# Performance work log

Hardware: AMD Instinct MI355X
Metric: run time of the kernel (lower is better)

The kernel has to match this reference:

```python
import jax, jax.numpy as jnp
import numpy as np


def setup_inputs() -> dict:
    key = jax.random.key(0)
    k1, k2, k3, k4 = jax.random.split(key, 4)
    B, T, C = 4, 2048, 1024
    x = jax.random.normal(k1, (B, T, C), dtype=jnp.float32)
    scale = 1.0 / np.sqrt(C)
    Wq = jax.random.normal(k2, (C, C), dtype=jnp.float32) * scale
    Wk = jax.random.normal(k3, (C, C), dtype=jnp.float32) * scale
    Wv = jax.random.normal(k4, (C, C), dtype=jnp.float32) * scale
    return {"x": x, "Wq": Wq, "Wk": Wk, "Wv": Wv}


def reference(x, Wq, Wk, Wv):
    # x: [B, T, C]; torch Linear(no bias): y = x @ W.T
    B, T, C = x.shape
    q = jnp.einsum('btc,dc->btd', x, Wq)
    k = jnp.einsum('btc,dc->btd', x, Wk)
    v = jnp.einsum('btc,dc->btd', x, Wv)
    scale = jnp.asarray(C, x.dtype) ** -0.5
    qk = jnp.einsum('bqd,bkd->bqk', q, k) * scale  # [B, T, T]
    causal = jnp.tril(jnp.ones((T, T), dtype=bool))
    qk = jnp.where(causal, qk, -jnp.inf)
    attn = jax.nn.softmax(qk, axis=-1)
    out = jnp.einsum('bqk,bkd->bqd', attn, v)
    return out
```

## Files before the change

kernel.cpp:

```cpp
#include <hip/hip_runtime.h>

typedef __attribute__((ext_vector_type(8))) short  short8;
typedef __attribute__((ext_vector_type(4))) short  short4v;
typedef __attribute__((ext_vector_type(4))) float  floatx4;

__device__ inline short f2bf(float f) {
    union { float f; unsigned u; } v; v.f = f;
    unsigned r = v.u + 0x7fffu + ((v.u >> 16) & 1u);
    return (short)(r >> 16);
}

typedef const __attribute__((address_space(1))) unsigned int* gp1_t;
typedef __attribute__((address_space(3))) unsigned int* lp3_t;

__device__ __attribute__((always_inline)) inline void gl_lds16(const short* g, short* l) {
    __builtin_amdgcn_global_load_lds((gp1_t)g, (lp3_t)l, 16, 0, 0);
}

#define MFMA_BF16 __builtin_amdgcn_mfma_f32_16x16x32_bf16

__device__ __attribute__((always_inline)) inline void gemm_bt_core(
    const short* __restrict__ Ag, const short* __restrict__ Bg,
    int lda, int ldb, int kmax,
    short* As, short* Bs, floatx4 acc[4][4])
{
    const int t    = threadIdx.x;
    const int srow = t >> 3;
    const int scol = (t & 7) * 8;
    const int lane = t & 63;
    const int wid  = t >> 6;
    const int wx   = wid & 1, wy = wid >> 1;
    const int lm   = lane & 15, lq = lane >> 4;

    for (int k0 = 0; k0 < kmax; k0 += 64) {
        __syncthreads();
#pragma unroll
        for (int i = 0; i < 4; ++i) {
            gl_lds16(Ag + (size_t)(i * 32 + srow) * lda + k0 + scol,
                     As + (i * 32 + srow) * 64 + scol);
            gl_lds16(Bg + (size_t)(i * 32 + srow) * ldb + k0 + scol,
                     Bs + (i * 32 + srow) * 64 + scol);
        }
        __syncthreads();

#pragma unroll
        for (int ks = 0; ks < 2; ++ks) {
            short8 af[4], bfr[4];
#pragma unroll
            for (int mi = 0; mi < 4; ++mi)
                af[mi] = *(const short8*)(As + (wy * 64 + mi * 16 + lm) * 64 + ks * 32 + lq * 8);
#pragma unroll
            for (int ni = 0; ni < 4; ++ni)
                bfr[ni] = *(const short8*)(Bs + (wx * 64 + ni * 16 + lm) * 64 + ks * 32 + lq * 8);
#pragma unroll
            for (int mi = 0; mi < 4; ++mi)
#pragma unroll
                for (int ni = 0; ni < 4; ++ni)
                    acc[mi][ni] = MFMA_BF16(af[mi], bfr[ni], acc[mi][ni], 0, 0, 0);
        }
    }
}

__global__ void cast_all(const float* __restrict__ x,
                         const float* __restrict__ Wq,
                         const float* __restrict__ Wk,
                         const float* __restrict__ Wv,
                         short* __restrict__ xb, short* __restrict__ wb,
                         float* __restrict__ lsum)
{
    size_t v = (size_t)blockIdx.x * 256 + threadIdx.x;
    const float* src; short* dst; size_t off;
    if (v < 2097152)      { src = x;  dst = xb;           off = v; }
    else if (v < 2359296) { src = Wq; dst = wb;           off = v - 2097152; }
    else if (v < 2621440) { src = Wk; dst = wb + 1048576; off = v - 2359296; }
    else if (v < 2883584) { src = Wv; dst = wb + 2097152; off = v - 2621440; }
    else if (v < 2885632) {
        floatx4 z = {0.f, 0.f, 0.f, 0.f};
        ((floatx4*)lsum)[v - 2883584] = z;
        return;
    } else return;
    floatx4 vv = ((const floatx4*)src)[off];
    short4v s;
#pragma unroll
    for (int e = 0; e < 4; ++e) s[e] = f2bf(vv[e]);
    ((short4v*)dst)[off] = s;
}

struct Q8Ctx {
    const short* Ag; const short* Bg;
    short *A0, *B0, *A1, *B1;
    int srow, scl, scg;
    int aB, bB, c0, c1;
};

#define LD_AF(SLOT, HI) do { _Pragma("unroll") \
    for (int mi_ = 0; mi_ < 4; ++mi_) { \
        af[mi_][0] = *(const short8*)((SLOT) + X.aB + (HI) + mi_ * 1024 + X.c0); \
        af[mi_][1] = *(const short8*)((SLOT) + X.aB + (HI) + mi_ * 1024 + X.c1); \
    } } while (0)

#define LD_BF(SLOT, N0) do { _Pragma("unroll") \
    for (int ni_ = 0; ni_ < 2; ++ni_) { \
        bf[(N0) + ni_][0] = *(const short8*)((SLOT) + X.bB + ((N0) + ni_) * 1024 + X.c0); \
        bf[(N0) + ni_][1] = *(const short8*)((SLOT) + X.bB + ((N0) + ni_) * 1024 + X.c1); \
    } } while (0)

#define MM_Q(MB, N0) do { _Pragma("unroll") \
    for (int mi_ = 0; mi_ < 4; ++mi_) { _Pragma("unroll") \
        for (int ni_ = 0; ni_ < 2; ++ni_) { \
            acc[(MB)+mi_][(N0)+ni_] = MFMA_BF16(af[mi_][0], bf[(N0)+ni_][0], acc[(MB)+mi_][(N0)+ni_], 0, 0, 0); \
            acc[(MB)+mi_][(N0)+ni_] = MFMA_BF16(af[mi_][1], bf[(N0)+ni_][1], acc[(MB)+mi_][(N0)+ni_], 0, 0, 0); \
        } } } while (0)

#define STAGE_HALF(DST, SRC, KOFS) do { \
    gl_lds16((SRC) + (size_t)(X.srow)      * 1024 + (KOFS) + X.scg, (DST) + (X.srow)      * 64 + X.scl); \
    gl_lds16((SRC) + (size_t)(64 + X.srow) * 1024 + (KOFS) + X.scg, (DST) + (64 + X.srow) * 64 + X.scl); \
    } while (0)

#define BARR  __builtin_amdgcn_s_barrier()
#define WLG0  asm volatile("s_waitcnt lgkmcnt(0)" ::: "memory")
#define WLG8  asm volatile("s_waitcnt lgkmcnt(8)" ::: "memory")
#define PRI1  __builtin_amdgcn_s_setprio(1)
#define PRI0  __builtin_amdgcn_s_setprio(0)

template<bool TAIL>
__device__ __attribute__((always_inline)) inline void iter8(
    const Q8Ctx& X, int kb, floatx4 acc[8][4])
{
    const int sk1 = kb + 64, sk2 = kb + 128, sk3 = kb + 192;
    short8 af[4][2], bf[4][2];

    LD_AF(X.A0, 0); LD_BF(X.B0, 0);
    STAGE_HALF(X.A1, X.Ag, sk1);
    WLG8;
    BARR; WLG0; PRI1; MM_Q(0, 0); PRI0; BARR;
    LD_BF(X.B0, 2);
    STAGE_HALF(X.A1 + 8192, X.Ag + 131072, sk1);
    BARR; WLG0; PRI1; MM_Q(0, 2); PRI0; BARR;
    LD_AF(X.A0, 4096);
    if (!TAIL) STAGE_HALF(X.B0, X.Bg, sk2);
    BARR; WLG0; PRI1; MM_Q(4, 2); PRI0; BARR;
    if (!TAIL) STAGE_HALF(X.B0 + 8192, X.Bg + 131072, sk2);
    BARR; PRI1; MM_Q(4, 0); PRI0;
    if (!TAIL) asm volatile("s_waitcnt vmcnt(4)" ::: "memory");
    else       asm volatile("s_waitcnt vmcnt(0)" ::: "memory");
    BARR;

    LD_AF(X.A1, 0); LD_BF(X.B1, 0);
    if (!TAIL) STAGE_HALF(X.A0, X.Ag, sk2);
    WLG8;
    BARR; WLG0; PRI1; MM_Q(0, 0); PRI0; BARR;
    LD_BF(X.B1, 2);
    if (!TAIL) STAGE_HALF(X.A0 + 8192, X.Ag + 131072, sk2);
    BARR; WLG0; PRI1; MM_Q(0, 2); PRI0; BARR;
    LD_AF(X.A1, 4096);
    if (!TAIL) STAGE_HALF(X.B1, X.Bg, sk3);
    BARR; WLG0; PRI1; MM_Q(4, 2); PRI0; BARR;
    if (!TAIL) STAGE_HALF(X.B1 + 8192, X.Bg + 131072, sk3);
    BARR; PRI1; MM_Q(4, 0); PRI0;
    if (!TAIL) asm volatile("s_waitcnt vmcnt(4)" ::: "memory");
    BARR;
}

__global__ __launch_bounds__(512, 2) void qkv_gemm8(
    const short* __restrict__ xb, const short* __restrict__ wb,
    short* __restrict__ qb, short* __restrict__ kb, short* __restrict__ vt)
{
    __shared__ short lds[65536];

    const int orig = blockIdx.x;
    const int tile = (orig & 7) * 48 + (orig >> 3);
    const int mt = tile & 31;
    const int nt = tile >> 5;
    const int m0 = mt * 256;

    const int t    = threadIdx.x;
    const int lane = t & 63;
    const int wid  = t >> 6;
    const int wy   = wid >> 2, wx = wid & 3;
    const int lm   = lane & 15, lq = lane >> 4;

    Q8Ctx X;
    X.Ag = xb + (size_t)m0 * 1024;
    X.Bg = wb + (size_t)(nt * 256) * 1024;
    X.A0 = lds;          X.B0 = lds + 16384;
    X.A1 = lds + 32768;  X.B1 = lds + 49152;
    X.srow = t >> 3;
    X.scl  = (t & 7) * 8;
    X.scg  = ((t & 7) ^ (X.srow & 7)) * 8;
    X.c0 = (lq ^ (lm & 7)) * 8;
    X.c1 = ((4 + lq) ^ (lm & 7)) * 8;
    X.aB = (wy * 128 + lm) * 64;
    X.bB = (wx * 64 + lm) * 64;

    floatx4 acc[8][4];
    floatx4 zero = {0.f, 0.f, 0.f, 0.f};
#pragma unroll
    for (int i = 0; i < 8; ++i)
#pragma unroll
        for (int j = 0; j < 4; ++j) acc[i][j] = zero;

    STAGE_HALF(X.A0,         X.Ag,          0);
    STAGE_HALF(X.A0 + 8192,  X.Ag + 131072, 0);
    STAGE_HALF(X.B0,         X.Bg,          0);
    STAGE_HALF(X.B0 + 8192,  X.Bg + 131072, 0);
    STAGE_HALF(X.B1,         X.Bg,          64);
    STAGE_HALF(X.B1 + 8192,  X.Bg + 131072, 64);
    asm volatile("s_waitcnt vmcnt(4)" ::: "memory");
    __builtin_amdgcn_s_barrier();

#pragma unroll 1
    for (int i = 0; i < 7; ++i)
        iter8<false>(X, i * 128, acc);
    iter8<true>(X, 7 * 128, acc);

    const int nglob = nt * 256;
    const int which = nglob >> 10;
    const int ncol  = (nglob & 1023) + wx * 64;
#pragma unroll
    for (int mi = 0; mi < 8; ++mi)
#pragma unroll
        for (int r = 0; r < 4; ++r) {
            const int row = m0 + wy * 128 + mi * 16 + lq * 4 + r;
#pragma unroll
            for (int ni = 0; ni < 4; ++ni) {
                const int col = ncol + ni * 16 + lm;
                const short bv = f2bf(acc[mi][ni][r]);
                if (which == 2) {
                    const int bb = row >> 11, tt = row & 2047;
                    vt[((size_t)bb * 1024 + col) * 2048 + tt] = bv;
                } else if (which == 1) {
                    kb[(size_t)row * 1024 + col] = bv;
                } else {
                    qb[(size_t)row * 1024 + col] = bv;
                }
            }
        }
}

__global__ __launch_bounds__(256, 3) void sqk_gemm(
    const short* __restrict__ qb, const short* __restrict__ kb,
    short* __restrict__ P, float* __restrict__ lsum)
{
    int idx = blockIdx.x;
    int i = 0;
    while ((i + 1) * (i + 2) / 2 <= idx) ++i;
    const int j = idx - i * (i + 1) / 2;
    const int b = blockIdx.y;

    __shared__ short As[128 * 64];
    __shared__ short Bs[128 * 64];

    floatx4 acc[4][4];
    floatx4 zero = {0.f, 0.f, 0.f, 0.f};
#pragma unroll
    for (int a = 0; a < 4; ++a)
#pragma unroll
        for (int c = 0; c < 4; ++c) acc[a][c] = zero;

    gemm_bt_core(qb + ((size_t)(b * 2048 + i * 128)) * 1024,
                 kb + ((size_t)(b * 2048 + j * 128)) * 1024,
                 1024, 1024, 1024, As, Bs, acc);

    const float sscl = 0.03125f * 1.44269504089f;
    const bool  diag = (i == j);
    const int lane = threadIdx.x & 63, wid = threadIdx.x >> 6;
    const int wx = wid & 1, wy = wid >> 1, lm = lane & 15, lq = lane >> 4;

#pragma unroll
    for (int mi = 0; mi < 4; ++mi)
#pragma unroll
        for (int r = 0; r < 4; ++r) {
            const int lrow = wy * 64 + mi * 16 + lq * 4 + r;
            const int grow = i * 128 + lrow;
            short* prow = P + ((size_t)b * 2048 + grow) * 2048 + j * 128;
            float rsum = 0.f;
#pragma unroll
            for (int ni = 0; ni < 4; ++ni) {
                const int lcol = wx * 64 + ni * 16 + lm;
                float p = exp2f(acc[mi][ni][r] * sscl);
                if (diag && lcol > lrow) p = 0.f;
                rsum += p;
                prow[lcol] = f2bf(p);
            }
#pragma unroll
            for (int off = 1; off < 16; off <<= 1) rsum += __shfl_xor(rsum, off);
            if (lm == 0) atomicAdd(lsum + b * 2048 + grow, rsum);
        }
}

__global__ __launch_bounds__(256, 3) void pv_gemm(
    const short* __restrict__ P, const short* __restrict__ vt,
    const float* __restrict__ lsum, float* __restrict__ out)
{
    const int x  = blockIdx.x;
    const int pr = blockIdx.y;
    const int b  = blockIdx.z;
    const int n0 = x * 64;

    __shared__ short As[128 * 64];
    __shared__ short Bs[64 * 64];

    const int t    = threadIdx.x;
    const int srow = t >> 3;
    const int scol = (t & 7) * 8;
    const int lane = t & 63;
    const int wid  = t >> 6;
    const int wx   = wid & 1, wy = wid >> 1;
    const int lm   = lane & 15, lq = lane >> 4;

    const short* Bg = vt + ((size_t)b * 1024 + n0) * 2048;

#pragma unroll
    for (int phase = 0; phase < 2; ++phase) {
        const int i    = phase ? (15 - pr) : pr;
        const int kmax = (i + 1) * 128;
        const short* Ag = P + ((size_t)b * 2048 + i * 128) * 2048;

        floatx4 acc[4][2];
        floatx4 zero = {0.f, 0.f, 0.f, 0.f};
#pragma unroll
        for (int a = 0; a < 4; ++a)
#pragma unroll
            for (int c = 0; c < 2; ++c) acc[a][c] = zero;

        for (int k0 = 0; k0 < kmax; k0 += 64) {
            __syncthreads();
#pragma unroll
            for (int q = 0; q < 4; ++q)
                gl_lds16(Ag + (size_t)(q * 32 + srow) * 2048 + k0 + scol,
                         As + (q * 32 + srow) * 64 + scol);
#pragma unroll
            for (int q = 0; q < 2; ++q)
                gl_lds16(Bg + (size_t)(q * 32 + srow) * 2048 + k0 + scol,
                         Bs + (q * 32 + srow) * 64 + scol);
            __syncthreads();

#pragma unroll
            for (int ks = 0; ks < 2; ++ks) {
                short8 af[4], bfr[2];
#pragma unroll
                for (int mi = 0; mi < 4; ++mi)
                    af[mi] = *(const short8*)(As + (wy * 64 + mi * 16 + lm) * 64 + ks * 32 + lq * 8);
#pragma unroll
                for (int ni = 0; ni < 2; ++ni)
                    bfr[ni] = *(const short8*)(Bs + (wx * 32 + ni * 16 + lm) * 64 + ks * 32 + lq * 8);
#pragma unroll
                for (int mi = 0; mi < 4; ++mi)
#pragma unroll
                    for (int ni = 0; ni < 2; ++ni)
                        acc[mi][ni] = MFMA_BF16(af[mi], bfr[ni], acc[mi][ni], 0, 0, 0);
            }
        }

#pragma unroll
        for (int mi = 0; mi < 4; ++mi)
#pragma unroll
            for (int r = 0; r < 4; ++r) {
                const int grow = b * 2048 + i * 128 + wy * 64 + mi * 16 + lq * 4 + r;
                const float li = 1.0f / lsum[grow];
#pragma unroll
                for (int ni = 0; ni < 2; ++ni)
                    out[(size_t)grow * 1024 + n0 + wx * 32 + ni * 16 + lm] =
                        acc[mi][ni][r] * li;
            }
    }
}

extern "C" void kernel_launch(void* const* d_in, const int* in_sizes, int n_in,
                              void* d_out, int out_size, void* d_ws, size_t ws_size,
                              hipStream_t stream)
{
    (void)in_sizes; (void)n_in; (void)out_size; (void)ws_size;
    const float* x  = (const float*)d_in[0];
    const float* Wq = (const float*)d_in[1];
    const float* Wk = (const float*)d_in[2];
    const float* Wv = (const float*)d_in[3];
    float* out = (float*)d_out;

    char* base = (char*)d_ws;
    short* xb   = (short*)(base);
    short* wb   = (short*)(base + 16777216);
    short* qb   = (short*)(base + 23068672);
    short* kb   = (short*)(base + 39845888);
    short* vt   = (short*)(base + 56623104);
    short* P    = (short*)(base + 73400320);
    float* lsum = (float*)(base + 107954176);

    cast_all<<<11272, 256, 0, stream>>>(x, Wq, Wk, Wv, xb, wb, lsum);
    qkv_gemm8<<<dim3(384), 512, 0, stream>>>(xb, wb, qb, kb, vt);
    sqk_gemm<<<dim3(136, 4), 256, 0, stream>>>(qb, kb, P, lsum);
    pv_gemm<<<dim3(16, 8, 4), 256, 0, stream>>>(P, vt, lsum, out);
}
```

Baseline: 282.5 us.

## Split-K PV GEMM with atomics and rework QKV GEMM A-tile prefetch schedule

The PV GEMM now uses 128x128 output tiles via the shared gemm_bt_core. Long causal row blocks (i>=8) are split into two K halves that combine with float atomicAdd, and short rows are written directly. The lower half of the output is zeroed in the cast kernel so the atomics have a clean target. The QKV GEMM schedule is also reordered so A tiles are prefetched two stages ahead alongside B, with the waitcnt values adjusted to match. This trades more atomic traffic and an extra output-zeroing pass for better load balance and larger tiles.

```diff
diff --git a/kernel.cpp b/kernel.cpp
--- a/kernel.cpp
+++ b/kernel.cpp
@@ -66,7 +66,7 @@
                          const float* __restrict__ Wk,
                          const float* __restrict__ Wv,
                          short* __restrict__ xb, short* __restrict__ wb,
-                         float* __restrict__ lsum)
+                         float* __restrict__ lsum, float* __restrict__ out)
 {
     size_t v = (size_t)blockIdx.x * 256 + threadIdx.x;
     const float* src; short* dst; size_t off;
@@ -78,6 +78,12 @@
         floatx4 z = {0.f, 0.f, 0.f, 0.f};
         ((floatx4*)lsum)[v - 2883584] = z;
         return;
+    } else if (v < 3934208) {
+        size_t u = v - 2885632;
+        size_t bb = u >> 18, r = u & 262143;
+        floatx4 z = {0.f, 0.f, 0.f, 0.f};
+        ((floatx4*)out)[(bb * 2048 + 1024) * 256 + r] = z;
+        return;
     } else return;
     floatx4 vv = ((const floatx4*)src)[off];
     short4v s;
@@ -123,42 +129,46 @@
 #define PRI1  __builtin_amdgcn_s_setprio(1)
 #define PRI0  __builtin_amdgcn_s_setprio(0)
 
-template<bool TAIL>
-__device__ __attribute__((always_inline)) inline void iter8(
+template<int MODE>
+__device__ __attribute__((always_inline)) inline void iter8d(
     const Q8Ctx& X, int kb, floatx4 acc[8][4])
 {
-    const int sk1 = kb + 64, sk2 = kb + 128, sk3 = kb + 192;
+    const int sk2 = kb + 128, sk3 = kb + 192;
     short8 af[4][2], bf[4][2];
 
     LD_AF(X.A0, 0); LD_BF(X.B0, 0);
-    STAGE_HALF(X.A1, X.Ag, sk1);
     WLG8;
     BARR; WLG0; PRI1; MM_Q(0, 0); PRI0; BARR;
     LD_BF(X.B0, 2);
-    STAGE_HALF(X.A1 + 8192, X.Ag + 131072, sk1);
     BARR; WLG0; PRI1; MM_Q(0, 2); PRI0; BARR;
     LD_AF(X.A0, 4096);
-    if (!TAIL) STAGE_HALF(X.B0, X.Bg, sk2);
+    if (MODE == 0) STAGE_HALF(X.B0, X.Bg, sk2);
     BARR; WLG0; PRI1; MM_Q(4, 2); PRI0; BARR;
-    if (!TAIL) STAGE_HALF(X.B0 + 8192, X.Bg + 131072, sk2);
+    if (MODE == 0) {
+        STAGE_HALF(X.B0 + 8192, X.Bg + 131072, sk2);
+        STAGE_HALF(X.A0,        X.Ag,          sk2);
+    }
     BARR; PRI1; MM_Q(4, 0); PRI0;
-    if (!TAIL) asm volatile("s_waitcnt vmcnt(4)" ::: "memory");
-    else       asm volatile("s_waitcnt vmcnt(0)" ::: "memory");
+    if (MODE == 0) asm volatile("s_waitcnt vmcnt(6)" ::: "memory");
+    else           asm volatile("s_waitcnt vmcnt(0)" ::: "memory");
     BARR;
 
     LD_AF(X.A1, 0); LD_BF(X.B1, 0);
-    if (!TAIL) STAGE_HALF(X.A0, X.Ag, sk2);
+    if (MODE == 0) STAGE_HALF(X.A0 + 8192, X.Ag + 131072, sk2);
     WLG8;
     BARR; WLG0; PRI1; MM_Q(0, 0); PRI0; BARR;
     LD_BF(X.B1, 2);
-    if (!TAIL) STAGE_HALF(X.A0 + 8192, X.Ag + 131072, sk2);
     BARR; WLG0; PRI1; MM_Q(0, 2); PRI0; BARR;
     LD_AF(X.A1, 4096);
-    if (!TAIL) STAGE_HALF(X.B1, X.Bg, sk3);
+    if (MODE == 0) STAGE_HALF(X.B1, X.Bg, sk3);
     BARR; WLG0; PRI1; MM_Q(4, 2); PRI0; BARR;
-    if (!TAIL) STAGE_HALF(X.B1 + 8192, X.Bg + 131072, sk3);
+    if (MODE == 0) {
+        STAGE_HALF(X.B1 + 8192, X.Bg + 131072, sk3);
+        STAGE_HALF(X.A1,        X.Ag,          sk3);
+        STAGE_HALF(X.A1 + 8192, X.Ag + 131072, sk3);
+    }
     BARR; PRI1; MM_Q(4, 0); PRI0;
-    if (!TAIL) asm volatile("s_waitcnt vmcnt(4)" ::: "memory");
+    if (MODE == 0) asm volatile("s_waitcnt vmcnt(8)" ::: "memory");
     BARR;
 }
 
@@ -200,19 +210,21 @@
 #pragma unroll
         for (int j = 0; j < 4; ++j) acc[i][j] = zero;
 
+    STAGE_HALF(X.B0,         X.Bg,          0);
+    STAGE_HALF(X.B0 + 8192,  X.Bg + 131072, 0);
     STAGE_HALF(X.A0,         X.Ag,          0);
     STAGE_HALF(X.A0 + 8192,  X.Ag + 131072, 0);
-    STAGE_HALF(X.B0,         X.Bg,          0);
-    STAGE_HALF(X.B0 + 8192,  X.Bg + 131072, 0);
     STAGE_HALF(X.B1,         X.Bg,          64);
     STAGE_HALF(X.B1 + 8192,  X.Bg + 131072, 64);
-    asm volatile("s_waitcnt vmcnt(4)" ::: "memory");
+    STAGE_HALF(X.A1,         X.Ag,          64);
+    STAGE_HALF(X.A1 + 8192,  X.Ag + 131072, 64);
+    asm volatile("s_waitcnt vmcnt(8)" ::: "memory");
     __builtin_amdgcn_s_barrier();
 
 #pragma unroll 1
     for (int i = 0; i < 7; ++i)
-        iter8<false>(X, i * 128, acc);
-    iter8<true>(X, 7 * 128, acc);
+        iter8d<0>(X, i * 128, acc);
+    iter8d<1>(X, 7 * 128, acc);
 
     const int nglob = nt * 256;
     const int which = nglob >> 10;
@@ -293,78 +305,55 @@
     const short* __restrict__ P, const short* __restrict__ vt,
     const float* __restrict__ lsum, float* __restrict__ out)
 {
-    const int x  = blockIdx.x;
-    const int pr = blockIdx.y;
+    const int id = blockIdx.x;
+    const int x  = blockIdx.y;
     const int b  = blockIdx.z;
-    const int n0 = x * 64;
+    int i, kbeg, kend;
+    bool single;
+    if (id < 8) {
+        i = id; kbeg = 0; kend = (i + 1) * 128; single = true;
+    } else {
+        const int id2 = id - 8;
+        i = 8 + (id2 >> 1);
+        const int c = id2 & 1;
+        kbeg = c ? 1024 : 0;
+        kend = c ? (i + 1) * 128 : 1024;
+        single = false;
+    }
+    const int n0 = x * 128;
 
     __shared__ short As[128 * 64];
-    __shared__ short Bs[64 * 64];
-
-    const int t    = threadIdx.x;
-    const int srow = t >> 3;
-    const int scol = (t & 7) * 8;
-    const int lane = t & 63;
-    const int wid  = t >> 6;
-    const int wx   = wid & 1, wy = wid >> 1;
-    const int lm   = lane & 15, lq = lane >> 4;
-
-    const short* Bg = vt + ((size_t)b * 1024 + n0) * 2048;
-
-#pragma unroll
-    for (int phase = 0; phase < 2; ++phase) {
-        const int i    = phase ? (15 - pr) : pr;
-        const int kmax = (i + 1) * 128;
-        const short* Ag = P + ((size_t)b * 2048 + i * 128) * 2048;
-
-        floatx4 acc[4][2];
-        floatx4 zero = {0.f, 0.f, 0.f, 0.f};
-#pragma unroll
-        for (int a = 0; a < 4; ++a)
-#pragma unroll
-            for (int c = 0; c < 2; ++c) acc[a][c] = zero;
-
-        for (int k0 = 0; k0 < kmax; k0 += 64) {
-            __syncthreads();
-#pragma unroll
-            for (int q = 0; q < 4; ++q)
-                gl_lds16(Ag + (size_t)(q * 32 + srow) * 2048 + k0 + scol,
-                         As + (q * 32 + srow) * 64 + scol);
-#pragma unroll
-            for (int q = 0; q < 2; ++q)
-                gl_lds16(Bg + (size_t)(q * 32 + srow) * 2048 + k0 + scol,
-                         Bs + (q * 32 + srow) * 64 + scol);
-            __syncthreads();
-
-#pragma unroll
-            for (int ks = 0; ks < 2; ++ks) {
-                short8 af[4], bfr[2];
-#pragma unroll
-                for (int mi = 0; mi < 4; ++mi)
-                    af[mi] = *(const short8*)(As + (wy * 64 + mi * 16 + lm) * 64 + ks * 32 + lq * 8);
-#pragma unroll
-                for (int ni = 0; ni < 2; ++ni)
-                    bfr[ni] = *(const short8*)(Bs + (wx * 32 + ni * 16 + lm) * 64 + ks * 32 + lq * 8);
-#pragma unroll
-                for (int mi = 0; mi < 4; ++mi)
-#pragma unroll
-                    for (int ni = 0; ni < 2; ++ni)
-                        acc[mi][ni] = MFMA_BF16(af[mi], bfr[ni], acc[mi][ni], 0, 0, 0);
+    __shared__ short Bs[128 * 64];
+
+    const short* Ag = P  + ((size_t)b * 2048 + i * 128) * 2048 + kbeg;
+    const short* Bg = vt + ((size_t)b * 1024 + n0) * 2048 + kbeg;
+
+    floatx4 acc[4][4];
+    floatx4 zero = {0.f, 0.f, 0.f, 0.f};
+#pragma unroll
+    for (int a = 0; a < 4; ++a)
+#pragma unroll
+        for (int c2 = 0; c2 < 4; ++c2) acc[a][c2] = zero;
+
+    gemm_bt_core(Ag, Bg, 2048, 2048, kend - kbeg, As, Bs, acc);
+
+    const int lane = threadIdx.x & 63, wid = threadIdx.x >> 6;
+    const int wx = wid & 1, wy = wid >> 1, lm = lane & 15, lq = lane >> 4;
+
+#pragma unroll
+    for (int mi = 0; mi < 4; ++mi)
+#pragma unroll
+        for (int r = 0; r < 4; ++r) {
+            const int grow = b * 2048 + i * 128 + wy * 64 + mi * 16 + lq * 4 + r;
+            const float li = 1.0f / lsum[grow];
+#pragma unroll
+            for (int ni = 0; ni < 4; ++ni) {
+                float* dst = out + (size_t)grow * 1024 + n0 + wx * 64 + ni * 16 + lm;
+                const float val = acc[mi][ni][r] * li;
+                if (single) *dst = val;
+                else        atomicAdd(dst, val);
             }
         }
-
-#pragma unroll
-        for (int mi = 0; mi < 4; ++mi)
-#pragma unroll
-            for (int r = 0; r < 4; ++r) {
-                const int grow = b * 2048 + i * 128 + wy * 64 + mi * 16 + lq * 4 + r;
-                const float li = 1.0f / lsum[grow];
-#pragma unroll
-                for (int ni = 0; ni < 2; ++ni)
-                    out[(size_t)grow * 1024 + n0 + wx * 32 + ni * 16 + lm] =
-                        acc[mi][ni][r] * li;
-            }
-    }
 }
 
 extern "C" void kernel_launch(void* const* d_in, const int* in_sizes, int n_in,
@@ -387,8 +376,8 @@
     short* P    = (short*)(base + 73400320);
     float* lsum = (float*)(base + 107954176);
 
-    cast_all<<<11272, 256, 0, stream>>>(x, Wq, Wk, Wv, xb, wb, lsum);
+    cast_all<<<15368, 256, 0, stream>>>(x, Wq, Wk, Wv, xb, wb, lsum, out);
     qkv_gemm8<<<dim3(384), 512, 0, stream>>>(xb, wb, qb, kb, vt);
     sqk_gemm<<<dim3(136, 4), 256, 0, stream>>>(qb, kb, P, lsum);
-    pv_gemm<<<dim3(16, 8, 4), 256, 0, stream>>>(P, vt, lsum, out);
-}
+    pv_gemm<<<dim3(24, 8, 4), 256, 0, stream>>>(P, vt, lsum, out);
+}
```

New measurement: 290.4 us. 2.8% more time.
